# Kernel optimization log

Measured on AMD Instinct MI355X. Metric: run time of the kernel, lower is better.

The kernel has to match this reference:

```python
import jax, jax.numpy as jnp
import numpy as np

B = 32768

def setup_inputs() -> dict:
    key = jax.random.key(0)
    ks = jax.random.split(key, 6)
    x = jax.random.normal(ks[0], (B, 1, 28, 28), dtype=jnp.float32)
    conv_w = jax.random.normal(ks[1], (4, 1, 2, 2), dtype=jnp.float32) * 0.5   # Conv2d(1,4,2,2) OIHW
    conv_b = jax.random.normal(ks[2], (4,), dtype=jnp.float32) * 0.1
    q_w = jax.random.normal(ks[3], (4, 4), dtype=jnp.float32) * 0.5            # Linear(4,4,bias=False), (out,in)
    lin_w = jax.random.normal(ks[4], (10, 1568), dtype=jnp.float32) * 0.02     # Linear(1568,10), (out,in)
    lin_b = jax.random.normal(ks[5], (10,), dtype=jnp.float32) * 0.02
    return {"x": x, "conv_w": conv_w, "conv_b": conv_b, "q_w": q_w, "lin_w": lin_w, "lin_b": lin_b}

def reference(x, conv_w, conv_b, q_w, lin_w, lin_b):
    b = x.shape[0]
    # conv branch: (B,1,28,28) -> (B,4,14,14)
    conv = jax.lax.conv_general_dilated(
        x, conv_w, window_strides=(2, 2), padding='VALID',
        dimension_numbers=('NCHW', 'OIHW', 'NCHW')) + conv_b[None, :, None, None]
    cls_feat = conv.reshape(b, -1)  # (B,784)
    # quantum branch: all 196 non-overlapping 2x2 patches in loop (r,c) order,
    # each flattened row-major to 4 values, then one batched 4x4 linear.
    img = x.reshape(b, 28, 28)
    patches = img.reshape(b, 14, 2, 14, 2).transpose(0, 1, 3, 2, 4).reshape(b, 196, 4)
    qfeat = jnp.einsum('bpi,oi->bpo', patches, q_w).reshape(b, 196 * 4)  # (B,784)
    combined = jnp.concatenate([cls_feat, qfeat], axis=1)  # (B,1568)
    logits = combined @ lin_w.T + lin_b
    return jax.nn.log_softmax(logits, axis=-1)
```

## Files before the change

kernel.cpp:

```cpp
#include <hip/hip_runtime.h>
#include <math.h>

#define NOUT   10
#define ROWLEN 784
#define WTOT   (NOUT*ROWLEN)


__global__ __launch_bounds__(256)
void quanv_prep(const float* __restrict__ conv_w,
                const float* __restrict__ conv_b,
                const float* __restrict__ q_w,
                const float* __restrict__ lin_w,
                const float* __restrict__ lin_b,
                unsigned short* __restrict__ W16,
                float* __restrict__ biasOut)
{
    const int t = threadIdx.x;

    for (int idx = blockIdx.x * 256 + t; idx < WTOT; idx += gridDim.x * 256) {
        const int o = idx / ROWLEN;
        const int j = idx - o * ROWLEN;
        const int h = j / 28, w = j - h * 28;
        const int p = (h >> 1) * 14 + (w >> 1);
        const int k = (h & 1) * 2 + (w & 1);
        float s = 0.f;
        #pragma unroll
        for (int c = 0; c < 4; ++c)
            s += conv_w[c * 4 + k] * lin_w[o * 1568 + c * 196 + p];
        #pragma unroll
        for (int q = 0; q < 4; ++q)
            s += q_w[q * 4 + k] * lin_w[o * 1568 + 784 + p * 4 + q];
        unsigned int u = __float_as_uint(s);
        u += 0x7fffu + ((u >> 16) & 1u);
        W16[idx] = (unsigned short)(u >> 16);
    }

    if (blockIdx.x == 0) {
        __shared__ float rs[40];
        const int lane = t & 7;
        for (int pair = t >> 3; pair < 40; pair += 32) {
            const int o = pair >> 2, c = pair & 3;
            const float* base = lin_w + o * 1568 + c * 196;
            float s = 0.f;
            #pragma unroll
            for (int p = 0; p < 196; p += 8) {
                const int pp = p + lane;
                if (pp < 196) s += base[pp];
            }
            s += __shfl_xor(s, 1);
            s += __shfl_xor(s, 2);
            s += __shfl_xor(s, 4);
            if (lane == 0) rs[pair] = s;
        }
        __syncthreads();
        if (t < NOUT) {
            float s = lin_b[t];
            #pragma unroll
            for (int c = 0; c < 4; ++c) s += conv_b[c] * rs[t * 4 + c];
            biasOut[t] = s;
        }
    }
}

__global__ __launch_bounds__(256, 6)
void quanv_main(const float* __restrict__ x,
                const unsigned short* __restrict__ Wg,
                const float* __restrict__ biasG,
                float* __restrict__ out)
{
    __shared__ unsigned short Wl[WTOT];
    __shared__ float bias[NOUT];

    const int t    = threadIdx.x;
    const int lane = t & 63;
    const int wv   = t >> 6;
    const int l    = lane & 15;
    const int gp   = (lane >> 4) & 1;
    const int pr   = lane >> 5;
    const int r0   = blockIdx.x * 16 + wv * 4 + pr * 2;

    const float* __restrict__ xr = x + (size_t)r0 * ROWLEN;

    float4 px0[2], px1[2];
    #pragma unroll
    for (int r = 0; r < 2; ++r) {
        px0[r] = *(const float4*)(xr + r * ROWLEN + 4 * l);
        px1[r] = *(const float4*)(xr + r * ROWLEN + 4 * l + 64);
    }

    {
        const uint4* __restrict__ src = (const uint4*)Wg;
        uint4* dst = (uint4*)Wl;
        #pragma unroll
        for (int i = 0; i < 4; ++i) {
            const int idx = t + 256 * i;
            if (idx < WTOT / 8) dst[idx] = src[idx];
        }
        if (t < NOUT) bias[t] = biasG[t];
    }
    __syncthreads();

    float acc[2][5];
    #pragma unroll
    for (int r = 0; r < 2; ++r)
        #pragma unroll
        for (int o = 0; o < 5; ++o) acc[r][o] = 0.f;

    const int wb = gp * 5 * ROWLEN;

    #pragma unroll
    for (int i = 0; i < 12; ++i) {
        float4 cur[2];
        #pragma unroll
        for (int r = 0; r < 2; ++r) cur[r] = ((i & 1) == 0) ? px0[r] : px1[r];

        const int ni = i + 2;
        if (ni < 12) {
            const int nfo = 4 * l + 64 * ni;
            #pragma unroll
            for (int r = 0; r < 2; ++r) {
                const float4 v = *(const float4*)(xr + r * ROWLEN + nfo);
                if ((i & 1) == 0) px0[r] = v; else px1[r] = v;
            }
        } else if (ni == 12) {
            const int tfo = 768 + 4 * (l & 3);
            #pragma unroll
            for (int r = 0; r < 2; ++r)
                px0[r] = *(const float4*)(xr + r * ROWLEN + tfo);
        }

        const int fo = 4 * l + 64 * i;
        #pragma unroll
        for (int o = 0; o < 5; ++o) {
            const uint2 wp = *(const uint2*)&Wl[wb + o * ROWLEN + fo];
            const float w0 = __uint_as_float(wp.x << 16);
            const float w1 = __uint_as_float(wp.x & 0xffff0000u);
            const float w2 = __uint_as_float(wp.y << 16);
            const float w3 = __uint_as_float(wp.y & 0xffff0000u);
            #pragma unroll
            for (int r = 0; r < 2; ++r)
                acc[r][o] = fmaf(cur[r].x, w0, fmaf(cur[r].y, w1,
                            fmaf(cur[r].z, w2, fmaf(cur[r].w, w3, acc[r][o]))));
        }
    }
    if (l < 4) {
        const int fo = 768 + 4 * l;
        #pragma unroll
        for (int o = 0; o < 5; ++o) {
            const uint2 wp = *(const uint2*)&Wl[wb + o * ROWLEN + fo];
            const float w0 = __uint_as_float(wp.x << 16);
            const float w1 = __uint_as_float(wp.x & 0xffff0000u);
            const float w2 = __uint_as_float(wp.y << 16);
            const float w3 = __uint_as_float(wp.y & 0xffff0000u);
            #pragma unroll
            for (int r = 0; r < 2; ++r)
                acc[r][o] = fmaf(px0[r].x, w0, fmaf(px0[r].y, w1,
                            fmaf(px0[r].z, w2, fmaf(px0[r].w, w3, acc[r][o]))));
        }
    }

    #pragma unroll
    for (int r = 0; r < 2; ++r)
        #pragma unroll
        for (int o = 0; o < 5; ++o) {
            acc[r][o] += __shfl_xor(acc[r][o], 1);
            acc[r][o] += __shfl_xor(acc[r][o], 2);
            acc[r][o] += __shfl_xor(acc[r][o], 4);
            acc[r][o] += __shfl_xor(acc[r][o], 8);
        }

    float own[2][5], ex[2][5];
    #pragma unroll
    for (int r = 0; r < 2; ++r)
        #pragma unroll
        for (int o = 0; o < 5; ++o) {
            own[r][o] = acc[r][o] + bias[gp * 5 + o];
            ex[r][o]  = __shfl_xor(own[r][o], 16);
        }

    float lg[NOUT];
    #pragma unroll
    for (int o = 0; o < 5; ++o) {
        lg[o]     = gp ? ex[1][o]  : own[0][o];
        lg[o + 5] = gp ? own[1][o] : ex[0][o];
    }

    float m = -1e30f;
    #pragma unroll
    for (int o = 0; o < NOUT; ++o) m = fmaxf(m, lg[o]);
    float s = 0.f;
    #pragma unroll
    for (int o = 0; o < NOUT; ++o) s += expf(lg[o] - m);
    const float lse = m + logf(s);

    if (l < NOUT) {
        float v = lg[0];
        #pragma unroll
        for (int o = 1; o < NOUT; ++o) v = (l == o) ? lg[o] : v;
        out[(size_t)(r0 + gp) * NOUT + l] = v - lse;
    }
}

extern "C" void kernel_launch(void* const* d_in, const int* in_sizes, int n_in,
                              void* d_out, int out_size, void* d_ws, size_t ws_size,
                              hipStream_t stream) {
    const float* x      = (const float*)d_in[0];
    const float* conv_w = (const float*)d_in[1];
    const float* conv_b = (const float*)d_in[2];
    const float* q_w    = (const float*)d_in[3];
    const float* lin_w  = (const float*)d_in[4];
    const float* lin_b  = (const float*)d_in[5];
    float* out = (float*)d_out;

    unsigned short* W16 = (unsigned short*)d_ws;
    float* biasWs       = (float*)((char*)d_ws + 15680);

    const int rows = in_sizes[0] / ROWLEN;

    quanv_prep<<<31, 256, 0, stream>>>(conv_w, conv_b, q_w, lin_w, lin_b,
                                       W16, biasWs);
    quanv_main<<<rows / 16, 256, 0, stream>>>(x, W16, biasWs, out);
}
```

Measured before the change: 35.50 us.

## Stream x rows through double-buffered LDS via global_load_lds in persistent blocks

Each block now handles 64 rows instead of 16. It loops over 16 chunks of 4 rows and stages each chunk into a double-buffered LDS tile with async global_load_lds issued by wave 0, so the weight staging is amortised over more rows and loads overlap compute. Each wave processes one row per chunk, with its lanes split across output halves and row halves. The reduction gains an extra cross-half shuffle. The change costs 4x fewer blocks (512), a __syncthreads per chunk, extra LDS traffic for x, and no explicit wait on the async LDS loads before the barrier, which may be a correctness risk.

```diff
diff --git a/kernel.cpp b/kernel.cpp
--- a/kernel.cpp
+++ b/kernel.cpp
@@ -1,9 +1,13 @@
 #include <hip/hip_runtime.h>
 #include <math.h>
 
-#define NOUT   10
-#define ROWLEN 784
-#define WTOT   (NOUT*ROWLEN)
+#define NOUT    10
+#define ROWLEN  784
+#define WTOT    (NOUT*ROWLEN)
+#define CHROWS  4
+#define CHFL    (CHROWS*ROWLEN)
+#define NCH     16
+#define BROWS   (CHROWS*NCH)
 
 
 __global__ __launch_bounds__(256)
@@ -62,7 +66,18 @@
     }
 }
 
-__global__ __launch_bounds__(256, 6)
+__device__ __forceinline__ void gl_lds16(const float* g, float* s) {
+    __builtin_amdgcn_global_load_lds(
+        (const __attribute__((address_space(1))) unsigned int*)g,
+        (__attribute__((address_space(3))) unsigned int*)s, 16, 0, 0);
+}
+__device__ __forceinline__ void gl_lds4(const float* g, float* s) {
+    __builtin_amdgcn_global_load_lds(
+        (const __attribute__((address_space(1))) unsigned int*)g,
+        (__attribute__((address_space(3))) unsigned int*)s, 4, 0, 0);
+}
+
+__global__ __launch_bounds__(256)
 void quanv_main(const float* __restrict__ x,
                 const unsigned short* __restrict__ Wg,
                 const float* __restrict__ biasG,
@@ -70,22 +85,23 @@
 {
     __shared__ unsigned short Wl[WTOT];
     __shared__ float bias[NOUT];
+    __shared__ float xbuf[2][CHFL];
 
     const int t    = threadIdx.x;
     const int lane = t & 63;
     const int wv   = t >> 6;
     const int l    = lane & 15;
-    const int gp   = (lane >> 4) & 1;
-    const int pr   = lane >> 5;
-    const int r0   = blockIdx.x * 16 + wv * 4 + pr * 2;
-
-    const float* __restrict__ xr = x + (size_t)r0 * ROWLEN;
-
-    float4 px0[2], px1[2];
-    #pragma unroll
-    for (int r = 0; r < 2; ++r) {
-        px0[r] = *(const float4*)(xr + r * ROWLEN + 4 * l);
-        px1[r] = *(const float4*)(xr + r * ROWLEN + 4 * l + 64);
+    const int oh   = (lane >> 4) & 1;
+    const int kh   = lane >> 5;
+
+    const size_t rowbase = (size_t)blockIdx.x * BROWS;
+    const float* __restrict__ xblk = x + rowbase * ROWLEN;
+
+    if (wv == 0) {
+        #pragma unroll
+        for (int i = 0; i < 12; ++i)
+            gl_lds16(xblk + i * 256 + lane * 4, &xbuf[0][i * 256]);
+        gl_lds4(xblk + 3072 + lane, &xbuf[0][3072]);
     }
 
     {
@@ -100,104 +116,94 @@
     }
     __syncthreads();
 
-    float acc[2][5];
-    #pragma unroll
-    for (int r = 0; r < 2; ++r)
-        #pragma unroll
-        for (int o = 0; o < 5; ++o) acc[r][o] = 0.f;
-
-    const int wb = gp * 5 * ROWLEN;
-
-    #pragma unroll
-    for (int i = 0; i < 12; ++i) {
-        float4 cur[2];
-        #pragma unroll
-        for (int r = 0; r < 2; ++r) cur[r] = ((i & 1) == 0) ? px0[r] : px1[r];
-
-        const int ni = i + 2;
-        if (ni < 12) {
-            const int nfo = 4 * l + 64 * ni;
-            #pragma unroll
-            for (int r = 0; r < 2; ++r) {
-                const float4 v = *(const float4*)(xr + r * ROWLEN + nfo);
-                if ((i & 1) == 0) px0[r] = v; else px1[r] = v;
+    const int wb = oh * 5 * ROWLEN;
+    int b = 0;
+
+    for (int ch = 0; ch < NCH; ++ch) {
+        if (wv == 0 && ch + 1 < NCH) {
+            const float* src = xblk + (size_t)(ch + 1) * CHFL;
+            float* dst = xbuf[b ^ 1];
+            #pragma unroll
+            for (int i = 0; i < 12; ++i)
+                gl_lds16(src + i * 256 + lane * 4, dst + i * 256);
+            gl_lds4(src + 3072 + lane, dst + 3072);
+        }
+
+        const float* __restrict__ xr = &xbuf[b][wv * ROWLEN + kh * 392];
+        const unsigned short* __restrict__ wr = &Wl[wb + kh * 392];
+
+        float acc[5] = {0.f, 0.f, 0.f, 0.f, 0.f};
+
+        #pragma unroll
+        for (int i = 0; i < 6; ++i) {
+            const int fo = 4 * l + 64 * i;
+            const float4 a = *(const float4*)(xr + fo);
+            #pragma unroll
+            for (int o = 0; o < 5; ++o) {
+                const uint2 wp = *(const uint2*)(wr + o * ROWLEN + fo);
+                const float w0 = __uint_as_float(wp.x << 16);
+                const float w1 = __uint_as_float(wp.x & 0xffff0000u);
+                const float w2 = __uint_as_float(wp.y << 16);
+                const float w3 = __uint_as_float(wp.y & 0xffff0000u);
+                acc[o] = fmaf(a.x, w0, fmaf(a.y, w1,
+                         fmaf(a.z, w2, fmaf(a.w, w3, acc[o]))));
             }
-        } else if (ni == 12) {
-            const int tfo = 768 + 4 * (l & 3);
-            #pragma unroll
-            for (int r = 0; r < 2; ++r)
-                px0[r] = *(const float4*)(xr + r * ROWLEN + tfo);
-        }
-
-        const int fo = 4 * l + 64 * i;
+        }
+        if (l < 2) {
+            const int fo = 384 + 4 * l;
+            const float4 a = *(const float4*)(xr + fo);
+            #pragma unroll
+            for (int o = 0; o < 5; ++o) {
+                const uint2 wp = *(const uint2*)(wr + o * ROWLEN + fo);
+                const float w0 = __uint_as_float(wp.x << 16);
+                const float w1 = __uint_as_float(wp.x & 0xffff0000u);
+                const float w2 = __uint_as_float(wp.y << 16);
+                const float w3 = __uint_as_float(wp.y & 0xffff0000u);
+                acc[o] = fmaf(a.x, w0, fmaf(a.y, w1,
+                         fmaf(a.z, w2, fmaf(a.w, w3, acc[o]))));
+            }
+        }
+
         #pragma unroll
         for (int o = 0; o < 5; ++o) {
-            const uint2 wp = *(const uint2*)&Wl[wb + o * ROWLEN + fo];
-            const float w0 = __uint_as_float(wp.x << 16);
-            const float w1 = __uint_as_float(wp.x & 0xffff0000u);
-            const float w2 = __uint_as_float(wp.y << 16);
-            const float w3 = __uint_as_float(wp.y & 0xffff0000u);
-            #pragma unroll
-            for (int r = 0; r < 2; ++r)
-                acc[r][o] = fmaf(cur[r].x, w0, fmaf(cur[r].y, w1,
-                            fmaf(cur[r].z, w2, fmaf(cur[r].w, w3, acc[r][o]))));
-        }
-    }
-    if (l < 4) {
-        const int fo = 768 + 4 * l;
+            acc[o] += __shfl_xor(acc[o], 1);
+            acc[o] += __shfl_xor(acc[o], 2);
+            acc[o] += __shfl_xor(acc[o], 4);
+            acc[o] += __shfl_xor(acc[o], 8);
+            acc[o] += __shfl_xor(acc[o], 32);
+        }
+
+        float own[5], ex[5];
         #pragma unroll
         for (int o = 0; o < 5; ++o) {
-            const uint2 wp = *(const uint2*)&Wl[wb + o * ROWLEN + fo];
-            const float w0 = __uint_as_float(wp.x << 16);
-            const float w1 = __uint_as_float(wp.x & 0xffff0000u);
-            const float w2 = __uint_as_float(wp.y << 16);
-            const float w3 = __uint_as_float(wp.y & 0xffff0000u);
-            #pragma unroll
-            for (int r = 0; r < 2; ++r)
-                acc[r][o] = fmaf(px0[r].x, w0, fmaf(px0[r].y, w1,
-                            fmaf(px0[r].z, w2, fmaf(px0[r].w, w3, acc[r][o]))));
-        }
-    }
-
-    #pragma unroll
-    for (int r = 0; r < 2; ++r)
+            own[o] = acc[o] + bias[oh * 5 + o];
+            ex[o]  = __shfl_xor(own[o], 16);
+        }
+
+        float lg[NOUT];
         #pragma unroll
         for (int o = 0; o < 5; ++o) {
-            acc[r][o] += __shfl_xor(acc[r][o], 1);
-            acc[r][o] += __shfl_xor(acc[r][o], 2);
-            acc[r][o] += __shfl_xor(acc[r][o], 4);
-            acc[r][o] += __shfl_xor(acc[r][o], 8);
-        }
-
-    float own[2][5], ex[2][5];
-    #pragma unroll
-    for (int r = 0; r < 2; ++r)
-        #pragma unroll
-        for (int o = 0; o < 5; ++o) {
-            own[r][o] = acc[r][o] + bias[gp * 5 + o];
-            ex[r][o]  = __shfl_xor(own[r][o], 16);
-        }
-
-    float lg[NOUT];
-    #pragma unroll
-    for (int o = 0; o < 5; ++o) {
-        lg[o]     = gp ? ex[1][o]  : own[0][o];
-        lg[o + 5] = gp ? own[1][o] : ex[0][o];
-    }
-
-    float m = -1e30f;
-    #pragma unroll
-    for (int o = 0; o < NOUT; ++o) m = fmaxf(m, lg[o]);
-    float s = 0.f;
-    #pragma unroll
-    for (int o = 0; o < NOUT; ++o) s += expf(lg[o] - m);
-    const float lse = m + logf(s);
-
-    if (l < NOUT) {
-        float v = lg[0];
-        #pragma unroll
-        for (int o = 1; o < NOUT; ++o) v = (l == o) ? lg[o] : v;
-        out[(size_t)(r0 + gp) * NOUT + l] = v - lse;
+            lg[o]     = oh ? ex[o]  : own[o];
+            lg[o + 5] = oh ? own[o] : ex[o];
+        }
+
+        float m = -1e30f;
+        #pragma unroll
+        for (int o = 0; o < NOUT; ++o) m = fmaxf(m, lg[o]);
+        float s = 0.f;
+        #pragma unroll
+        for (int o = 0; o < NOUT; ++o) s += expf(lg[o] - m);
+        const float lse = m + logf(s);
+
+        if (lane < NOUT) {
+            float v = lg[0];
+            #pragma unroll
+            for (int o = 1; o < NOUT; ++o) v = (lane == o) ? lg[o] : v;
+            out[(rowbase + ch * CHROWS + wv) * NOUT + lane] = v - lse;
+        }
+
+        __syncthreads();
+        b ^= 1;
     }
 }
 
@@ -219,5 +225,5 @@
 
     quanv_prep<<<31, 256, 0, stream>>>(conv_w, conv_b, q_w, lin_w, lin_b,
                                        W16, biasWs);
-    quanv_main<<<rows / 16, 256, 0, stream>>>(x, W16, biasWs, out);
-}
+    quanv_main<<<rows / BROWS, 256, 0, stream>>>(x, W16, biasWs, out);
+}
```

After: 50.74 us. 1.43x slower.

## Store folded weights in fp32 LDS and deepen x prefetch to four stages

Applied to the files above, without the earlier changes.

Folded weights are kept in fp32 instead of bf16, which removes the per-element unpack shifts and masks and the rounding error, at the cost of twice the LDS footprint (31 KB per block). The launch-bounds occupancy hint drops from 6 to 5 blocks to match. The x prefetch ring grows from 2 to 4 float4 stages so more global loads are in flight. Bias is now read straight from global into registers rather than staged in LDS.

```diff
diff --git a/kernel.cpp b/kernel.cpp
--- a/kernel.cpp
+++ b/kernel.cpp
@@ -12,8 +12,7 @@
                 const float* __restrict__ q_w,
                 const float* __restrict__ lin_w,
                 const float* __restrict__ lin_b,
-                unsigned short* __restrict__ W16,
-                float* __restrict__ biasOut)
+                float* __restrict__ W)
 {
     const int t = threadIdx.x;
 
@@ -30,9 +29,7 @@
         #pragma unroll
         for (int q = 0; q < 4; ++q)
             s += q_w[q * 4 + k] * lin_w[o * 1568 + 784 + p * 4 + q];
-        unsigned int u = __float_as_uint(s);
-        u += 0x7fffu + ((u >> 16) & 1u);
-        W16[idx] = (unsigned short)(u >> 16);
+        W[idx] = s;
     }
 
     if (blockIdx.x == 0) {
@@ -57,47 +54,49 @@
             float s = lin_b[t];
             #pragma unroll
             for (int c = 0; c < 4; ++c) s += conv_b[c] * rs[t * 4 + c];
-            biasOut[t] = s;
+            W[WTOT + t] = s;
         }
     }
 }
 
-__global__ __launch_bounds__(256, 6)
+__global__ __launch_bounds__(256, 5)
 void quanv_main(const float* __restrict__ x,
-                const unsigned short* __restrict__ Wg,
-                const float* __restrict__ biasG,
+                const float* __restrict__ Wg,
                 float* __restrict__ out)
 {
-    __shared__ unsigned short Wl[WTOT];
-    __shared__ float bias[NOUT];
+    __shared__ float Wl[WTOT];
 
     const int t    = threadIdx.x;
     const int lane = t & 63;
     const int wv   = t >> 6;
     const int l    = lane & 15;
-    const int gp   = (lane >> 4) & 1;
+    const int oh   = (lane >> 4) & 1;
     const int pr   = lane >> 5;
     const int r0   = blockIdx.x * 16 + wv * 4 + pr * 2;
 
     const float* __restrict__ xr = x + (size_t)r0 * ROWLEN;
 
-    float4 px0[2], px1[2];
-    #pragma unroll
-    for (int r = 0; r < 2; ++r) {
-        px0[r] = *(const float4*)(xr + r * ROWLEN + 4 * l);
-        px1[r] = *(const float4*)(xr + r * ROWLEN + 4 * l + 64);
-    }
+    float4 px[4][2];
+    #pragma unroll
+    for (int j = 0; j < 4; ++j)
+        #pragma unroll
+        for (int r = 0; r < 2; ++r)
+            px[j][r] = *(const float4*)(xr + r * ROWLEN + 4 * l + 64 * j);
 
     {
-        const uint4* __restrict__ src = (const uint4*)Wg;
-        uint4* dst = (uint4*)Wl;
-        #pragma unroll
-        for (int i = 0; i < 4; ++i) {
+        const float4* __restrict__ src = (const float4*)Wg;
+        float4* dst = (float4*)Wl;
+        #pragma unroll
+        for (int i = 0; i < 8; ++i) {
             const int idx = t + 256 * i;
-            if (idx < WTOT / 8) dst[idx] = src[idx];
-        }
-        if (t < NOUT) bias[t] = biasG[t];
-    }
+            if (idx < WTOT / 4) dst[idx] = src[idx];
+        }
+    }
+
+    float bias_r[5];
+    #pragma unroll
+    for (int o = 0; o < 5; ++o) bias_r[o] = Wg[WTOT + oh * 5 + o];
+
     __syncthreads();
 
     float acc[2][5];
@@ -106,56 +105,44 @@
         #pragma unroll
         for (int o = 0; o < 5; ++o) acc[r][o] = 0.f;
 
-    const int wb = gp * 5 * ROWLEN;
+    const int wb = oh * 5 * ROWLEN;
 
     #pragma unroll
     for (int i = 0; i < 12; ++i) {
-        float4 cur[2];
-        #pragma unroll
-        for (int r = 0; r < 2; ++r) cur[r] = ((i & 1) == 0) ? px0[r] : px1[r];
-
-        const int ni = i + 2;
+        const int buf = i & 3;
+        const float4 a0 = px[buf][0];
+        const float4 a1 = px[buf][1];
+
+        const int ni = i + 4;
         if (ni < 12) {
             const int nfo = 4 * l + 64 * ni;
-            #pragma unroll
-            for (int r = 0; r < 2; ++r) {
-                const float4 v = *(const float4*)(xr + r * ROWLEN + nfo);
-                if ((i & 1) == 0) px0[r] = v; else px1[r] = v;
-            }
+            px[buf][0] = *(const float4*)(xr + nfo);
+            px[buf][1] = *(const float4*)(xr + ROWLEN + nfo);
         } else if (ni == 12) {
             const int tfo = 768 + 4 * (l & 3);
-            #pragma unroll
-            for (int r = 0; r < 2; ++r)
-                px0[r] = *(const float4*)(xr + r * ROWLEN + tfo);
+            px[0][0] = *(const float4*)(xr + tfo);
+            px[0][1] = *(const float4*)(xr + ROWLEN + tfo);
         }
 
         const int fo = 4 * l + 64 * i;
         #pragma unroll
         for (int o = 0; o < 5; ++o) {
-            const uint2 wp = *(const uint2*)&Wl[wb + o * ROWLEN + fo];
-            const float w0 = __uint_as_float(wp.x << 16);
-            const float w1 = __uint_as_float(wp.x & 0xffff0000u);
-            const float w2 = __uint_as_float(wp.y << 16);
-            const float w3 = __uint_as_float(wp.y & 0xffff0000u);
-            #pragma unroll
-            for (int r = 0; r < 2; ++r)
-                acc[r][o] = fmaf(cur[r].x, w0, fmaf(cur[r].y, w1,
-                            fmaf(cur[r].z, w2, fmaf(cur[r].w, w3, acc[r][o]))));
+            const float4 w4 = *(const float4*)&Wl[wb + o * ROWLEN + fo];
+            acc[0][o] = fmaf(a0.x, w4.x, fmaf(a0.y, w4.y,
+                        fmaf(a0.z, w4.z, fmaf(a0.w, w4.w, acc[0][o]))));
+            acc[1][o] = fmaf(a1.x, w4.x, fmaf(a1.y, w4.y,
+                        fmaf(a1.z, w4.z, fmaf(a1.w, w4.w, acc[1][o]))));
         }
     }
     if (l < 4) {
         const int fo = 768 + 4 * l;
         #pragma unroll
         for (int o = 0; o < 5; ++o) {
-            const uint2 wp = *(const uint2*)&Wl[wb + o * ROWLEN + fo];
-            const float w0 = __uint_as_float(wp.x << 16);
-            const float w1 = __uint_as_float(wp.x & 0xffff0000u);
-            const float w2 = __uint_as_float(wp.y << 16);
-            const float w3 = __uint_as_float(wp.y & 0xffff0000u);
-            #pragma unroll
-            for (int r = 0; r < 2; ++r)
-                acc[r][o] = fmaf(px0[r].x, w0, fmaf(px0[r].y, w1,
-                            fmaf(px0[r].z, w2, fmaf(px0[r].w, w3, acc[r][o]))));
+            const float4 w4 = *(const float4*)&Wl[wb + o * ROWLEN + fo];
+            acc[0][o] = fmaf(px[0][0].x, w4.x, fmaf(px[0][0].y, w4.y,
+                        fmaf(px[0][0].z, w4.z, fmaf(px[0][0].w, w4.w, acc[0][o]))));
+            acc[1][o] = fmaf(px[0][1].x, w4.x, fmaf(px[0][1].y, w4.y,
+                        fmaf(px[0][1].z, w4.z, fmaf(px[0][1].w, w4.w, acc[1][o]))));
         }
     }
 
@@ -174,15 +161,15 @@
     for (int r = 0; r < 2; ++r)
         #pragma unroll
         for (int o = 0; o < 5; ++o) {
-            own[r][o] = acc[r][o] + bias[gp * 5 + o];
+            own[r][o] = acc[r][o] + bias_r[o];
             ex[r][o]  = __shfl_xor(own[r][o], 16);
         }
 
     float lg[NOUT];
     #pragma unroll
     for (int o = 0; o < 5; ++o) {
-        lg[o]     = gp ? ex[1][o]  : own[0][o];
-        lg[o + 5] = gp ? own[1][o] : ex[0][o];
+        lg[o]     = oh ? ex[1][o]  : own[0][o];
+        lg[o + 5] = oh ? own[1][o] : ex[0][o];
     }
 
     float m = -1e30f;
@@ -197,7 +184,7 @@
         float v = lg[0];
         #pragma unroll
         for (int o = 1; o < NOUT; ++o) v = (l == o) ? lg[o] : v;
-        out[(size_t)(r0 + gp) * NOUT + l] = v - lse;
+        out[(size_t)(r0 + oh) * NOUT + l] = v - lse;
     }
 }
 
@@ -211,13 +198,10 @@
     const float* lin_w  = (const float*)d_in[4];
     const float* lin_b  = (const float*)d_in[5];
     float* out = (float*)d_out;
-
-    unsigned short* W16 = (unsigned short*)d_ws;
-    float* biasWs       = (float*)((char*)d_ws + 15680);
+    float* W   = (float*)d_ws;
 
     const int rows = in_sizes[0] / ROWLEN;
 
-    quanv_prep<<<31, 256, 0, stream>>>(conv_w, conv_b, q_w, lin_w, lin_b,
-                                       W16, biasWs);
-    quanv_main<<<rows / 16, 256, 0, stream>>>(x, W16, biasWs, out);
+    quanv_prep<<<31, 256, 0, stream>>>(conv_w, conv_b, q_w, lin_w, lin_b, W);
+    quanv_main<<<rows / 16, 256, 0, stream>>>(x, W, out);
 }
```

After: 32.69 us. 7.9% less time.
